# Performance work log

Hardware: AMD Instinct MI355X
Metric: run time of the kernel (lower is better)

Reference implementation:

```python
import jax, jax.numpy as jnp
import numpy as np

B, SEQ, DIM = 32, 512, 1024
DEPTH, HEADS, DHEAD = 6, 8, 64
INNER = HEADS * DHEAD  # 512
NLAT, MAXSEQ = 64, 512
EPS = 1e-5


def setup_inputs() -> dict:
    key = jax.random.key(0)
    ks = jax.random.split(key, 8)
    return {
        "x": jax.random.normal(ks[0], (B, SEQ, DIM), dtype=jnp.float32),
        "attention_mask": jax.random.randint(ks[1], (B, SEQ), 0, 2, dtype=jnp.int32),
        "latents": jax.random.normal(ks[2], (NLAT, DIM), dtype=jnp.float32),
        "media_pos_emb": jax.random.normal(ks[3], (MAXSEQ, DIM), dtype=jnp.float32),
        "ln_media_g": jnp.ones((DEPTH, DIM), jnp.float32),
        "ln_media_b": jnp.zeros((DEPTH, DIM), jnp.float32),
        "ln_lat_g": jnp.ones((DEPTH, DIM), jnp.float32),
        "ln_lat_b": jnp.zeros((DEPTH, DIM), jnp.float32),
        "Wq": jax.random.normal(ks[4], (DEPTH, DIM, INNER), dtype=jnp.float32) * 0.02,
        "Wkv": jax.random.normal(ks[5], (DEPTH, DIM, 2 * INNER), dtype=jnp.float32) * 0.02,
        "Wout": jax.random.normal(ks[6], (DEPTH, INNER, DIM), dtype=jnp.float32) * 0.02,
        "final_g": jnp.ones((DIM,), jnp.float32),
        "final_b": jnp.zeros((DIM,), jnp.float32),
    }


def _layer_norm(x, g, b):
    mu = jnp.mean(x, axis=-1, keepdims=True)
    var = jnp.mean(jnp.square(x - mu), axis=-1, keepdims=True)
    return (x - mu) * jax.lax.rsqrt(var + EPS) * g + b


def _heads(t):
    # b n (h d) -> b h n d
    b, n, _ = t.shape
    return t.reshape(b, n, HEADS, DHEAD).transpose(0, 2, 1, 3)


def reference(x, attention_mask, latents, media_pos_emb, ln_media_g, ln_media_b,
              ln_lat_g, ln_lat_b, Wq, Wkv, Wout, final_g, final_b):
    b, seq, _ = x.shape
    x = x + media_pos_emb[None, :seq, :]
    lat = jnp.broadcast_to(latents[None], (b, NLAT, DIM))
    scale = DHEAD ** -0.5
    # key mask over [latents ++ media]: latent keys never masked; 1 == masked
    key_mask = jnp.concatenate(
        [jnp.zeros((b, NLAT), attention_mask.dtype), attention_mask], axis=1)
    masked = (key_mask == 1)[:, None, None, :]  # b 1 1 j
    for l in range(DEPTH):
        xm = _layer_norm(x, ln_media_g[l], ln_media_b[l])
        ln = _layer_norm(lat, ln_lat_g[l], ln_lat_b[l])
        q = _heads(ln @ Wq[l])                      # b h i d
        kv = jnp.concatenate([ln, xm], axis=1) @ Wkv[l]
        k, v = jnp.split(kv, 2, axis=-1)
        k, v = _heads(k), _heads(v)                 # b h j d
        sim = jnp.einsum('bhid,bhjd->bhij', q * scale, k)
        sim = jnp.where(masked, -jnp.inf, sim)
        attn = jax.nn.softmax(sim, axis=-1)
        out = jnp.einsum('bhij,bhjd->bhid', attn, v)
        out = out.transpose(0, 2, 1, 3).reshape(b, NLAT, INNER)
        lat = lat + out @ Wout[l]
    return _layer_norm(lat, final_g, final_b)
```

## Files before the change

### kernel.cpp

```cpp
#include <hip/hip_runtime.h>
#include <cstdint>


#define DEVINL __device__ __forceinline__

typedef __attribute__((ext_vector_type(8))) short short8_t;
typedef __attribute__((ext_vector_type(4))) float f32x4;

DEVINL ushort f2bf(float f) {
  union { float f; uint32_t u; } c; c.f = f;
  uint32_t u = c.u;
  u += ((u >> 16) & 1u) + 0x7fffu;
  return (ushort)(u >> 16);
}
DEVINL float bf2f(ushort u) {
  union { uint32_t u; float f; } c; c.u = ((uint32_t)u) << 16;
  return c.f;
}
DEVINL f32x4 mfma16(short8_t a, short8_t b, f32x4 c) {
  return __builtin_amdgcn_mfma_f32_16x16x32_bf16(a, b, c, 0, 0, 0);
}
DEVINL void gld16(ushort* lds, const ushort* g) {
  __builtin_amdgcn_global_load_lds(
      (const __attribute__((address_space(1))) void*)g,
      (__attribute__((address_space(3))) void*)lds, 16, 0, 0);
}

__global__ __launch_bounds__(512, 2) void k_gemm256m(const ushort* __restrict__ A,
    const ushort* __restrict__ Bt, const float* __restrict__ bias,
    ushort* __restrict__ Kb, ushort* __restrict__ Vt) {
  extern __shared__ char lds[];
  constexpr int K = 1024, NT = 16;
  int tid = threadIdx.x, lane = tid & 63, w = tid >> 6;
  int wm = w >> 2, wn = w & 3;
  int fr = lane & 15;
  int fkb = (lane >> 4) << 4;
  int xorv = (fr & 7) << 4;
  int bid = blockIdx.x;
  int xcd = bid & 7, ii = bid >> 3;
  int m0 = (xcd * 8 + (ii >> 2)) * 256;
  int n0 = (ii & 3) * 256;
  int srow = w * 8 + (lane >> 3);
  int sce = ((lane & 7) ^ (lane >> 3)) << 3;
  const ushort* Ag = A + (size_t)(m0 + srow) * K + sce;
  const ushort* Bg = Bt + (size_t)(n0 + srow) * K + sce;
  f32x4 acc[8][4] = {};

  auto stA = [&](int t, int h) {
    ushort* d = (ushort*)(lds + (t % 3) * 32768 + h * 16384 + w * 1024);
    const ushort* s = Ag + (size_t)(h * 128) * K + t * 64;
    gld16(d, s);
    gld16((ushort*)((char*)d + 8192), s + (size_t)64 * K);
  };
  auto stB = [&](int t, int h) {
    ushort* d = (ushort*)(lds + 98304 + (t & 1) * 32768 + h * 16384 + w * 1024);
    const ushort* s = Bg + (size_t)(h * 128) * K + t * 64;
    gld16(d, s);
    gld16((ushort*)((char*)d + 8192), s + (size_t)64 * K);
  };
  stA(0, 0); stA(0, 1); stB(0, 0); stB(0, 1); stA(1, 0); stA(1, 1);

#define RD_AFR(DST, MQ)                                                        \
  _Pragma("unroll") for (int m2 = 0; m2 < 2; ++m2)                             \
    _Pragma("unroll") for (int kh = 0; kh < 2; ++kh)                           \
      DST[m2][kh] = *(const short8_t*)(ab +                                    \
          ((wm * 128 + (MQ + m2) * 16 + fr) << 7) + ((kh * 64 + fkb) ^ xorv));

#define CLUSTER(MQ, AFR)                                                       \
  __builtin_amdgcn_s_setprio(1);                                               \
  _Pragma("unroll") for (int kh = 0; kh < 2; ++kh)                             \
    _Pragma("unroll") for (int m2 = 0; m2 < 2; ++m2)                           \
      _Pragma("unroll") for (int nt = 0; nt < 4; ++nt)                         \
        acc[MQ + m2][nt] = mfma16(AFR[m2][kh], bfr[nt][kh], acc[MQ + m2][nt]); \
  __builtin_amdgcn_s_setprio(0);                                               \
  __builtin_amdgcn_s_barrier();

  for (int t = 0; t < NT; ++t) {
    const char* ab = lds + (t % 3) * 32768;
    const char* bb = lds + 98304 + (t & 1) * 32768;
    short8_t bfr[4][2], afrX[2][2], afrY[2][2];
    if (t + 1 < NT) asm volatile("s_waitcnt vmcnt(4)" ::: "memory");
    else            asm volatile("s_waitcnt vmcnt(0)" ::: "memory");
    __builtin_amdgcn_s_barrier();
#pragma unroll
    for (int nt = 0; nt < 4; ++nt)
#pragma unroll
      for (int kh = 0; kh < 2; ++kh)
        bfr[nt][kh] = *(const short8_t*)(bb +
            ((wn * 64 + nt * 16 + fr) << 7) + ((kh * 64 + fkb) ^ xorv));
    RD_AFR(afrX, 0);
    if (t + 1 < NT) stB(t + 1, 0);
    RD_AFR(afrY, 2);
    CLUSTER(0, afrX);
    if (t + 1 < NT) stB(t + 1, 1);
    RD_AFR(afrX, 4);
    CLUSTER(2, afrY);
    if (t + 2 < NT) stA(t + 2, 0);
    RD_AFR(afrY, 6);
    CLUSTER(4, afrX);
    if (t + 2 < NT) stA(t + 2, 1);
    CLUSTER(6, afrY);
  }
#undef RD_AFR
#undef CLUSTER

  __syncthreads();
  ushort* Cl = (ushort*)lds;
  constexpr int CLS = 264;
  for (int p = 0; p < 2; ++p) {
    if (p) __syncthreads();
    if (wm == p) {
#pragma unroll
      for (int mt = 0; mt < 8; ++mt)
#pragma unroll
        for (int nt = 0; nt < 4; ++nt)
#pragma unroll
          for (int r = 0; r < 4; ++r) {
            int rl = mt * 16 + ((lane >> 4) << 2) + r;
            int cl = wn * 64 + nt * 16 + (lane & 15);
            Cl[rl * CLS + cl] = f2bf(acc[mt][nt][r] + bias[n0 + cl]);
          }
    }
    __syncthreads();
    int rowg0 = m0 + p * 128;
    int b_ = rowg0 >> 9;
    int jbase = 64 + (rowg0 & 511);
    if (n0 < 512) {
#pragma unroll
      for (int q2 = 0; q2 < 8; ++q2) {
        int task = tid + q2 * 512;
        int rl = task >> 5, ck = task & 31;
        short8_t vv = *(const short8_t*)&Cl[rl * CLS + ck * 8];
        *(short8_t*)&Kb[((size_t)(b_ * 576 + jbase + rl) << 9) + n0 + ck * 8] = vv;
      }
    } else {
#pragma unroll
      for (int q2 = 0; q2 < 8; ++q2) {
        int task = tid + q2 * 512;
        int d = task >> 4, jg = task & 15;
        short8_t vv;
#pragma unroll
        for (int e = 0; e < 8; ++e) vv[e] = (short)Cl[(jg * 8 + e) * CLS + d];
        *(short8_t*)&Vt[((size_t)(b_ * 512 + (n0 - 512) + d)) * 576 +
                        jbase + jg * 8] = vv;
      }
    }
  }
}

__global__ __launch_bounds__(256) void k_fold_kv(const float* __restrict__ Wkv,
    const float* __restrict__ lnmg, const float* __restrict__ lnlg,
    const float* __restrict__ lnmb, const float* __restrict__ lnlb,
    ushort* __restrict__ wkvmT, ushort* __restrict__ wlatT,
    float* __restrict__ bkvm, float* __restrict__ blat) {
  __shared__ float tile[32][33];
  __shared__ float pm[8][32], pl[8][32];
  int l = blockIdx.y;
  int c0 = blockIdx.x * 32;
  const float* Wl = Wkv + (size_t)l * 1048576;
  int tx = threadIdx.x & 31, ty = threadIdx.x >> 5;
  float am = 0.f, al = 0.f;
  for (int rt = 0; rt < 32; ++rt) {
    int r0 = rt * 32;
    __syncthreads();
#pragma unroll
    for (int i = 0; i < 4; ++i)
      tile[ty + i * 8][tx] = Wl[(size_t)(r0 + ty + i * 8) * 1024 + c0 + tx];
    __syncthreads();
#pragma unroll
    for (int i = 0; i < 4; ++i) {
      int r = ty * 4 + i;
      float wv = tile[r][tx];
      am += lnmb[l * 1024 + r0 + r] * wv;
      al += lnlb[l * 1024 + r0 + r] * wv;
    }
#pragma unroll
    for (int i = 0; i < 4; ++i) {
      int c = ty + i * 8;
      float wv = tile[tx][c];
      int r = r0 + tx;
      wkvmT[(size_t)l * 1048576 + (size_t)(c0 + c) * 1024 + r] =
          f2bf(wv * lnmg[l * 1024 + r]);
      wlatT[(size_t)l * 1572864 + (size_t)(512 + c0 + c) * 1024 + r] =
          f2bf(wv * lnlg[l * 1024 + r]);
    }
  }
  pm[ty][tx] = am; pl[ty][tx] = al;
  __syncthreads();
  if (ty == 0) {
    float sm = 0.f, sl = 0.f;
#pragma unroll
    for (int k = 0; k < 8; ++k) { sm += pm[k][tx]; sl += pl[k][tx]; }
    bkvm[l * 1024 + c0 + tx] = sm;
    blat[l * 1536 + 512 + c0 + tx] = sl;
  }
}

__global__ __launch_bounds__(256) void k_fold_q(const float* __restrict__ Wq,
    const float* __restrict__ lnlg, const float* __restrict__ lnlb,
    ushort* __restrict__ wlatT, float* __restrict__ blat) {
  __shared__ float tile[32][33];
  __shared__ float pq[8][32];
  int l = blockIdx.y;
  int c0 = blockIdx.x * 32;
  const float* Wl = Wq + (size_t)l * 524288;
  int tx = threadIdx.x & 31, ty = threadIdx.x >> 5;
  float aq = 0.f;
  for (int rt = 0; rt < 32; ++rt) {
    int r0 = rt * 32;
    __syncthreads();
#pragma unroll
    for (int i = 0; i < 4; ++i)
      tile[ty + i * 8][tx] = Wl[(size_t)(r0 + ty + i * 8) * 512 + c0 + tx];
    __syncthreads();
#pragma unroll
    for (int i = 0; i < 4; ++i) {
      int r = ty * 4 + i;
      aq += lnlb[l * 1024 + r0 + r] * tile[r][tx];
    }
#pragma unroll
    for (int i = 0; i < 4; ++i) {
      int c = ty + i * 8;
      float wv = tile[tx][c];
      int r = r0 + tx;
      wlatT[(size_t)l * 1572864 + (size_t)(c0 + c) * 1024 + r] =
          f2bf(wv * lnlg[l * 1024 + r] * 0.125f);
    }
  }
  pq[ty][tx] = aq;
  __syncthreads();
  if (ty == 0) {
    float s = 0.f;
#pragma unroll
    for (int k = 0; k < 8; ++k) s += pq[k][tx];
    blat[l * 1536 + c0 + tx] = s * 0.125f;
  }
}

__global__ __launch_bounds__(256) void k_fold_out(const float* __restrict__ Wout,
    ushort* __restrict__ woutT) {
  __shared__ float tile[32][33];
  int l = blockIdx.z;
  const float* Wl = Wout + (size_t)l * 524288;
  int r0 = blockIdx.y * 32, c0 = blockIdx.x * 32;
  int tx = threadIdx.x & 31, ty = threadIdx.x >> 5;
#pragma unroll
  for (int i = 0; i < 4; ++i)
    tile[ty + i * 8][tx] = Wl[(size_t)(r0 + ty + i * 8) * 1024 + c0 + tx];
  __syncthreads();
#pragma unroll
  for (int i = 0; i < 4; ++i) {
    int jl = ty + i * 8;
    woutT[(size_t)l * 524288 + (size_t)(c0 + jl) * 512 + r0 + tx] = f2bf(tile[tx][jl]);
  }
}

__global__ __launch_bounds__(256) void k_rownorm(const float* __restrict__ in,
    const float* __restrict__ pos, ushort* __restrict__ out) {
  int row = blockIdx.x, t = threadIdx.x;
  float4 v = *(const float4*)(in + (size_t)row * 1024 + t * 4);
  if (pos) {
    float4 p = *(const float4*)(pos + (size_t)(row & 511) * 1024 + t * 4);
    v.x += p.x; v.y += p.y; v.z += p.z; v.w += p.w;
  }
  float s = v.x + v.y + v.z + v.w;
  float q = v.x * v.x + v.y * v.y + v.z * v.z + v.w * v.w;
#pragma unroll
  for (int off = 32; off; off >>= 1) { s += __shfl_xor(s, off); q += __shfl_xor(q, off); }
  __shared__ float rs[4], rq[4];
  if ((t & 63) == 0) { rs[t >> 6] = s; rq[t >> 6] = q; }
  __syncthreads();
  s = rs[0] + rs[1] + rs[2] + rs[3];
  q = rq[0] + rq[1] + rq[2] + rq[3];
  float mean = s * (1.0f / 1024.0f);
  float var = q * (1.0f / 1024.0f) - mean * mean;
  float rstd = rsqrtf(var + 1e-5f);
  ushort4 o;
  o.x = f2bf((v.x - mean) * rstd);
  o.y = f2bf((v.y - mean) * rstd);
  o.z = f2bf((v.z - mean) * rstd);
  o.w = f2bf((v.w - mean) * rstd);
  *(ushort4*)(out + (size_t)row * 1024 + t * 4) = o;
}

__global__ __launch_bounds__(256) void k_finalln(const float* __restrict__ in,
    const float* __restrict__ g, const float* __restrict__ b, float* __restrict__ out) {
  int row = blockIdx.x, t = threadIdx.x;
  float4 v = *(const float4*)(in + (size_t)row * 1024 + t * 4);
  float s = v.x + v.y + v.z + v.w;
  float q = v.x * v.x + v.y * v.y + v.z * v.z + v.w * v.w;
#pragma unroll
  for (int off = 32; off; off >>= 1) { s += __shfl_xor(s, off); q += __shfl_xor(q, off); }
  __shared__ float rs[4], rq[4];
  if ((t & 63) == 0) { rs[t >> 6] = s; rq[t >> 6] = q; }
  __syncthreads();
  s = rs[0] + rs[1] + rs[2] + rs[3];
  q = rq[0] + rq[1] + rq[2] + rq[3];
  float mean = s * (1.0f / 1024.0f);
  float var = q * (1.0f / 1024.0f) - mean * mean;
  float rstd = rsqrtf(var + 1e-5f);
  float4 g4 = *(const float4*)(g + t * 4);
  float4 b4 = *(const float4*)(b + t * 4);
  float4 o;
  o.x = (v.x - mean) * rstd * g4.x + b4.x;
  o.y = (v.y - mean) * rstd * g4.y + b4.y;
  o.z = (v.z - mean) * rstd * g4.z + b4.z;
  o.w = (v.w - mean) * rstd * g4.w + b4.w;
  *(float4*)(out + (size_t)row * 1024 + t * 4) = o;
}

__global__ __launch_bounds__(256) void k_latinit(const float* __restrict__ latents,
                                                 float* __restrict__ lat) {
  int row = blockIdx.x, t = threadIdx.x;
  *(float4*)(lat + (size_t)row * 1024 + t * 4) =
      *(const float4*)(latents + (size_t)(row & 63) * 1024 + t * 4);
}

template <int MODE>
__global__ __launch_bounds__(256) void k_gemm64(const ushort* __restrict__ A,
    const ushort* __restrict__ Bt, const float* __restrict__ bias,
    ushort* __restrict__ o0, ushort* __restrict__ o1, ushort* __restrict__ o2,
    float* __restrict__ of, int N, int K) {
  __shared__ ushort Al[2][64][32];
  __shared__ ushort Bl[2][64][32];
  __shared__ ushort Cl[64][72];
  int tid = threadIdx.x, lane = tid & 63, w = tid >> 6;
  int wr = w >> 1, wc = w & 1;
  int m0 = blockIdx.y * 64, n0 = blockIdx.x * 64;
  f32x4 acc[2][2] = {};
  const ushort* Ag = A + (size_t)(m0 + w * 16 + (lane >> 2)) * K + (lane & 3) * 8;
  const ushort* Bg = Bt + (size_t)(n0 + w * 16 + (lane >> 2)) * K + (lane & 3) * 8;
  int fr = lane & 15, fk = (lane >> 4) << 3;
  int nt = K >> 5;
  gld16(&Al[0][w * 16][0], Ag);
  gld16(&Bl[0][w * 16][0], Bg);
  __syncthreads();
  for (int t = 0; t < nt; ++t) {
    int cur = t & 1;
    if (t + 1 < nt) {
      int k0 = (t + 1) << 5;
      gld16(&Al[cur ^ 1][w * 16][0], Ag + k0);
      gld16(&Bl[cur ^ 1][w * 16][0], Bg + k0);
    }
    short8_t a[2], b[2];
#pragma unroll
    for (int mt = 0; mt < 2; ++mt)
      a[mt] = *(const short8_t*)&Al[cur][wr * 32 + mt * 16 + fr][fk];
#pragma unroll
    for (int nt2 = 0; nt2 < 2; ++nt2)
      b[nt2] = *(const short8_t*)&Bl[cur][wc * 32 + nt2 * 16 + fr][fk];
#pragma unroll
    for (int mt = 0; mt < 2; ++mt)
#pragma unroll
      for (int nt2 = 0; nt2 < 2; ++nt2)
        acc[mt][nt2] = mfma16(a[mt], b[nt2], acc[mt][nt2]);
    __syncthreads();
  }
  if constexpr (MODE == 3) {
    if (n0 >= 1024) {
#pragma unroll
      for (int mt = 0; mt < 2; ++mt)
#pragma unroll
        for (int nt2 = 0; nt2 < 2; ++nt2)
#pragma unroll
          for (int r = 0; r < 4; ++r) {
            int rl = wr * 32 + mt * 16 + ((lane >> 4) << 2) + r;
            int col = wc * 32 + nt2 * 16 + (lane & 15);
            Cl[rl][col] = f2bf(acc[mt][nt2][r] + bias[n0 + col]);
          }
      __syncthreads();
      int b_ = m0 >> 6;
#pragma unroll
      for (int q = 0; q < 2; ++q) {
        int task = tid + q * 256;
        int jg = task & 7, d = task >> 3;
        short8_t vv;
#pragma unroll
        for (int e = 0; e < 8; ++e) vv[e] = (short)Cl[jg * 8 + e][d];
        *(short8_t*)&o2[((size_t)(b_ * 512 + (n0 - 1024) + d)) * 576 + jg * 8] = vv;
      }
      return;
    }
  }
#pragma unroll
  for (int mt = 0; mt < 2; ++mt)
#pragma unroll
    for (int nt2 = 0; nt2 < 2; ++nt2)
#pragma unroll
      for (int r = 0; r < 4; ++r) {
        int row = m0 + wr * 32 + mt * 16 + ((lane >> 4) << 2) + r;
        int col = n0 + wc * 32 + nt2 * 16 + (lane & 15);
        float v = acc[mt][nt2][r] + (bias ? bias[col] : 0.0f);
        if constexpr (MODE == 3) {
          int b_ = row >> 6, ii = row & 63;
          if (col < 512) o0[(size_t)row * 512 + col] = f2bf(v);
          else           o1[(((size_t)(b_ * 576 + ii)) << 9) + (col - 512)] = f2bf(v);
        } else {
          of[(size_t)row * N + col] += v;
        }
      }
}

__global__ __launch_bounds__(256) void k_attn(const ushort* __restrict__ Q,
    const ushort* __restrict__ Kb, const ushort* __restrict__ Vt,
    const int* __restrict__ amask, ushort* __restrict__ AO) {
  __shared__ ushort sim[32][584];
  int blk = blockIdx.x;
  int half = blk & 1, h = (blk >> 1) & 7, b = blk >> 4;
  int tid = threadIdx.x, lane = tid & 63, w = tid >> 6;
  int wr = w >> 1, wc = w & 1;
  short8_t aq0, aq1;
  {
    int qi = half * 32 + wr * 16 + (lane & 15);
    const ushort* qp = Q + ((size_t)(b * 64 + qi) << 9) + h * 64 + ((lane >> 4) << 3);
    aq0 = *(const short8_t*)qp;
    aq1 = *(const short8_t*)(qp + 32);
  }
  const ushort* kbase = Kb + (((size_t)(b * 576)) << 9) + h * 64 + ((lane >> 4) << 3);
  for (int jt = 0; jt < 9; ++jt) {
#pragma unroll
    for (int c2 = 0; c2 < 2; ++c2) {
      int ct = wc * 2 + c2;
      const ushort* kp = kbase + (((size_t)(jt * 64 + ct * 16 + (lane & 15))) << 9);
      short8_t bk0 = *(const short8_t*)kp;
      short8_t bk1 = *(const short8_t*)(kp + 32);
      f32x4 acc = {};
      acc = mfma16(aq0, bk0, acc);
      acc = mfma16(aq1, bk1, acc);
#pragma unroll
      for (int r = 0; r < 4; ++r)
        sim[wr * 16 + ((lane >> 4) << 2) + r][jt * 64 + ct * 16 + (lane & 15)] =
            f2bf(acc[r]);
    }
  }
  __syncthreads();
  unsigned mbits = 0;
#pragma unroll
  for (int c = 1; c < 9; ++c)
    if (amask[b * 512 + (c - 1) * 64 + lane]) mbits |= (1u << c);
  for (int rr = 0; rr < 8; ++rr) {
    int row = w * 8 + rr;
    float vals[9];
    float m = -3.0e38f;
#pragma unroll
    for (int c = 0; c < 9; ++c) {
      float v = bf2f(sim[row][c * 64 + lane]);
      vals[c] = v;
      if (!((mbits >> c) & 1)) m = fmaxf(m, v);
    }
#pragma unroll
    for (int off = 32; off; off >>= 1) m = fmaxf(m, __shfl_xor(m, off));
    float ssum = 0.f;
    float p[9];
#pragma unroll
    for (int c = 0; c < 9; ++c) {
      p[c] = ((mbits >> c) & 1) ? 0.f : __expf(vals[c] - m);
      ssum += p[c];
    }
#pragma unroll
    for (int off = 32; off; off >>= 1) ssum += __shfl_xor(ssum, off);
    float inv = 1.0f / ssum;
#pragma unroll
    for (int c = 0; c < 9; ++c)
      sim[row][c * 64 + lane] = f2bf(p[c] * inv);
  }
  __syncthreads();
  f32x4 oacc[2] = {};
  const ushort* vbase = Vt + ((size_t)(b * 512 + h * 64)) * 576 + ((lane >> 4) << 3);
  for (int jt = 0; jt < 9; ++jt) {
    short8_t pa0 = *(const short8_t*)&sim[wr * 16 + (lane & 15)][jt * 64 + ((lane >> 4) << 3)];
    short8_t pa1 = *(const short8_t*)&sim[wr * 16 + (lane & 15)][jt * 64 + 32 + ((lane >> 4) << 3)];
#pragma unroll
    for (int d2 = 0; d2 < 2; ++d2) {
      int dt = wc * 2 + d2;
      const ushort* vp = vbase + (size_t)(dt * 16 + (lane & 15)) * 576 + jt * 64;
      short8_t bv0 = *(const short8_t*)vp;
      short8_t bv1 = *(const short8_t*)(vp + 32);
      oacc[d2] = mfma16(pa0, bv0, oacc[d2]);
      oacc[d2] = mfma16(pa1, bv1, oacc[d2]);
    }
  }
#pragma unroll
  for (int d2 = 0; d2 < 2; ++d2) {
    int dt = wc * 2 + d2;
#pragma unroll
    for (int r = 0; r < 4; ++r) {
      int i = half * 32 + wr * 16 + ((lane >> 4) << 2) + r;
      int d = dt * 16 + (lane & 15);
      AO[((size_t)(b * 64 + i) << 9) + h * 64 + d] = f2bf(oacc[d2][r]);
    }
  }
}

extern "C" void kernel_launch(void* const* d_in, const int* in_sizes, int n_in,
                              void* d_out, int out_size, void* d_ws, size_t ws_size,
                              hipStream_t stream) {
  const float* x       = (const float*)d_in[0];
  const int*   amask   = (const int*)d_in[1];
  const float* latents = (const float*)d_in[2];
  const float* pos     = (const float*)d_in[3];
  const float* lnmg    = (const float*)d_in[4];
  const float* lnmb    = (const float*)d_in[5];
  const float* lnlg    = (const float*)d_in[6];
  const float* lnlb    = (const float*)d_in[7];
  const float* Wq      = (const float*)d_in[8];
  const float* Wkv     = (const float*)d_in[9];
  const float* Wout    = (const float*)d_in[10];
  const float* fg      = (const float*)d_in[11];
  const float* fb      = (const float*)d_in[12];
  float* out = (float*)d_out;
  char* ws = (char*)d_ws;

  ushort* xhat  = (ushort*)(ws + 0);
  ushort* wkvmT = (ushort*)(ws + 33554432);
  ushort* wlatT = (ushort*)(ws + 46137344);
  ushort* woutT = (ushort*)(ws + 65011712);
  float*  bkvm  = (float*)(ws + 71303168);
  float*  blat  = (float*)(ws + 71327744);
  float*  lat   = (float*)(ws + 71364608);
  ushort* lhat  = (ushort*)(ws + 79753216);
  ushort* qbuf  = (ushort*)(ws + 83947520);
  ushort* Kbuf  = (ushort*)(ws + 86044672);
  ushort* Vt    = (ushort*)(ws + 104919040);
  ushort* aobuf = (ushort*)(ws + 123793408);

  (void)hipFuncSetAttribute((const void*)k_gemm256m,
                            hipFuncAttributeMaxDynamicSharedMemorySize, 163840);

  dim3 B256(256);
  k_fold_kv<<<dim3(32, 6), B256, 0, stream>>>(Wkv, lnmg, lnlg, lnmb, lnlb,
                                              wkvmT, wlatT, bkvm, blat);
  k_fold_q<<<dim3(16, 6), B256, 0, stream>>>(Wq, lnlg, lnlb, wlatT, blat);
  k_fold_out<<<dim3(32, 16, 6), B256, 0, stream>>>(Wout, woutT);
  k_rownorm<<<16384, B256, 0, stream>>>(x, pos, xhat);
  k_latinit<<<2048, B256, 0, stream>>>(latents, lat);

  for (int l = 0; l < 6; ++l) {
    k_rownorm<<<2048, B256, 0, stream>>>(lat, nullptr, lhat);
    k_gemm64<3><<<dim3(24, 32), B256, 0, stream>>>(
        lhat, wlatT + (size_t)l * 1572864, blat + l * 1536,
        qbuf, Kbuf, Vt, nullptr, 1536, 1024);
    k_gemm256m<<<dim3(256), dim3(512), 163840, stream>>>(
        xhat, wkvmT + (size_t)l * 1048576, bkvm + l * 1024, Kbuf, Vt);
    k_attn<<<512, B256, 0, stream>>>(qbuf, Kbuf, Vt, amask, aobuf);
    k_gemm64<2><<<dim3(16, 32), B256, 0, stream>>>(
        aobuf, woutT + (size_t)l * 524288, nullptr,
        nullptr, nullptr, nullptr, lat, 1024, 512);
  }
  k_finalln<<<2048, B256, 0, stream>>>(lat, fg, fb, out);
}
```

Baseline: 737.9 us.

## Stage K/V through swizzled LDS with double buffering in attention, single-pass GEMM epilogue

The attention kernel now runs one 512-thread block per (batch, head) instead of splitting query rows across two blocks. K and V tiles are staged into XOR-swizzled shared memory with async global-to-LDS loads, double buffered so loads overlap the MFMA work. This removes the duplicated K/V global reads and the strided per-lane loads of the old version. Separately, the KV GEMM epilogue writes the whole 256-row tile to LDS in one pass, transposing on the write for V instead of on the read, which halves the barriers and makes V stores contiguous. In exchange, grid size drops to 256 blocks and each block uses about 121 KB of LDS, which lowers occupancy.

```diff
diff --git a/kernel.cpp b/kernel.cpp
--- a/kernel.cpp
+++ b/kernel.cpp
@@ -107,45 +107,170 @@
   __syncthreads();
   ushort* Cl = (ushort*)lds;
   constexpr int CLS = 264;
-  for (int p = 0; p < 2; ++p) {
-    if (p) __syncthreads();
-    if (wm == p) {
-#pragma unroll
-      for (int mt = 0; mt < 8; ++mt)
-#pragma unroll
-        for (int nt = 0; nt < 4; ++nt)
-#pragma unroll
-          for (int r = 0; r < 4; ++r) {
-            int rl = mt * 16 + ((lane >> 4) << 2) + r;
-            int cl = wn * 64 + nt * 16 + (lane & 15);
-            Cl[rl * CLS + cl] = f2bf(acc[mt][nt][r] + bias[n0 + cl]);
-          }
-    }
-    __syncthreads();
-    int rowg0 = m0 + p * 128;
-    int b_ = rowg0 >> 9;
-    int jbase = 64 + (rowg0 & 511);
-    if (n0 < 512) {
-#pragma unroll
-      for (int q2 = 0; q2 < 8; ++q2) {
-        int task = tid + q2 * 512;
-        int rl = task >> 5, ck = task & 31;
-        short8_t vv = *(const short8_t*)&Cl[rl * CLS + ck * 8];
-        *(short8_t*)&Kb[((size_t)(b_ * 576 + jbase + rl) << 9) + n0 + ck * 8] = vv;
+  bool isV = (n0 >= 512);
+#pragma unroll
+  for (int mt = 0; mt < 8; ++mt)
+#pragma unroll
+    for (int nt = 0; nt < 4; ++nt)
+#pragma unroll
+      for (int r = 0; r < 4; ++r) {
+        int rl = wm * 128 + mt * 16 + ((lane >> 4) << 2) + r;
+        int cl = wn * 64 + nt * 16 + fr;
+        ushort v = f2bf(acc[mt][nt][r] + bias[n0 + cl]);
+        if (!isV) Cl[rl * CLS + cl] = v;
+        else      Cl[cl * CLS + rl] = v;
       }
+  __syncthreads();
+  int b_ = m0 >> 9;
+  int jb = 64 + (m0 & 511);
+#pragma unroll
+  for (int q2 = 0; q2 < 16; ++q2) {
+    int task = tid + q2 * 512;
+    int rr2 = task >> 5, c8 = task & 31;
+    short8_t vv = *(const short8_t*)&Cl[rr2 * CLS + c8 * 8];
+    if (!isV)
+      *(short8_t*)&Kb[((size_t)(b_ * 576 + jb + rr2) << 9) + n0 + c8 * 8] = vv;
+    else
+      *(short8_t*)&Vt[(size_t)(b_ * 512 + (n0 - 512) + rr2) * 576 + jb + c8 * 8] = vv;
+  }
+}
+
+__global__ __launch_bounds__(512) void k_attn(const ushort* __restrict__ Q,
+    const ushort* __restrict__ Kb, const ushort* __restrict__ Vt,
+    const int* __restrict__ amask, ushort* __restrict__ AO) {
+  extern __shared__ char alds[];
+  ushort* sim = (ushort*)alds;
+  char* stg = alds + 74752;
+  int bh = blockIdx.x;
+  int h = bh & 7, b = bh >> 3;
+  int tid = threadIdx.x, lane = tid & 63, w = tid >> 6;
+  int rg = w >> 1, ch = w & 1;
+  int fr = lane & 15;
+  int fkb = (lane >> 4) << 4;
+  int csrc8 = ((lane & 7) ^ (lane >> 3)) << 3;
+  short8_t aq0, aq1;
+  {
+    int qi = rg * 16 + fr;
+    const ushort* qp = Q + ((size_t)(b * 64 + qi) << 9) + h * 64 + ((lane >> 4) << 3);
+    aq0 = *(const short8_t*)qp;
+    aq1 = *(const short8_t*)(qp + 32);
+  }
+  unsigned mbits = 0;
+#pragma unroll
+  for (int c = 1; c < 9; ++c)
+    if (amask[b * 512 + (c - 1) * 64 + lane]) mbits |= (1u << c);
+
+  auto stageK = [&](int it, int buf) {
+#pragma unroll
+    for (int g = 0; g < 3; ++g) {
+      int sr = w * 24 + g * 8 + (lane >> 3);
+      ushort* d = (ushort*)(stg + buf * 24576 + (w * 24 + g * 8) * 128);
+      gld16(d, Kb + ((size_t)(b * 576 + it * 192 + sr) << 9) + h * 64 + csrc8);
+    }
+  };
+  auto stageV = [&](int it, int buf) {
+#pragma unroll
+    for (int g = 0; g < 3; ++g) {
+      int sr = w * 8 + (lane >> 3);
+      ushort* d = (ushort*)(stg + buf * 24576 + g * 8192 + w * 8 * 128);
+      gld16(d, Vt + (size_t)(b * 512 + h * 64 + sr) * 576 + it * 192 + g * 64 + csrc8);
+    }
+  };
+
+  stageK(0, 0);
+  for (int it = 0; it < 3; ++it) {
+    int buf = it & 1;
+    __builtin_amdgcn_s_barrier();
+    if (it + 1 < 3) {
+      stageK(it + 1, buf ^ 1);
+      asm volatile("s_waitcnt vmcnt(3)" ::: "memory");
     } else {
-#pragma unroll
-      for (int q2 = 0; q2 < 8; ++q2) {
-        int task = tid + q2 * 512;
-        int d = task >> 4, jg = task & 15;
-        short8_t vv;
-#pragma unroll
-        for (int e = 0; e < 8; ++e) vv[e] = (short)Cl[(jg * 8 + e) * CLS + d];
-        *(short8_t*)&Vt[((size_t)(b_ * 512 + (n0 - 512) + d)) * 576 +
-                        jbase + jg * 8] = vv;
+      asm volatile("s_waitcnt vmcnt(0)" ::: "memory");
+    }
+    __builtin_amdgcn_s_barrier();
+    const char* kb_ = stg + buf * 24576;
+#pragma unroll
+    for (int ct = 0; ct < 6; ++ct) {
+      int row_l = ch * 96 + ct * 16 + fr;
+      const char* base = kb_ + row_l * 128;
+      int sw = (row_l & 7) << 4;
+      short8_t k0 = *(const short8_t*)(base + (fkb ^ sw));
+      short8_t k1 = *(const short8_t*)(base + ((64 + fkb) ^ sw));
+      f32x4 s4 = {};
+      s4 = mfma16(aq0, k0, s4);
+      s4 = mfma16(aq1, k1, s4);
+#pragma unroll
+      for (int r = 0; r < 4; ++r)
+        sim[(rg * 16 + ((lane >> 4) << 2) + r) * 584 +
+            it * 192 + ch * 96 + ct * 16 + fr] = f2bf(s4[r]);
+    }
+  }
+  __syncthreads();
+  for (int rr = 0; rr < 8; ++rr) {
+    int row = w * 8 + rr;
+    float vals[9];
+    float m = -3.0e38f;
+#pragma unroll
+    for (int c = 0; c < 9; ++c) {
+      float v = bf2f(sim[row * 584 + c * 64 + lane]);
+      vals[c] = v;
+      if (!((mbits >> c) & 1)) m = fmaxf(m, v);
+    }
+#pragma unroll
+    for (int off = 32; off; off >>= 1) m = fmaxf(m, __shfl_xor(m, off));
+    float ssum = 0.f;
+    float p[9];
+#pragma unroll
+    for (int c = 0; c < 9; ++c) {
+      p[c] = ((mbits >> c) & 1) ? 0.f : __expf(vals[c] - m);
+      ssum += p[c];
+    }
+#pragma unroll
+    for (int off = 32; off; off >>= 1) ssum += __shfl_xor(ssum, off);
+    float inv = 1.0f / ssum;
+#pragma unroll
+    for (int c = 0; c < 9; ++c)
+      sim[row * 584 + c * 64 + lane] = f2bf(p[c] * inv);
+  }
+  __syncthreads();
+  f32x4 oacc[2] = {};
+  stageV(0, 0);
+  for (int it = 0; it < 3; ++it) {
+    int buf = it & 1;
+    __builtin_amdgcn_s_barrier();
+    if (it + 1 < 3) {
+      stageV(it + 1, buf ^ 1);
+      asm volatile("s_waitcnt vmcnt(3)" ::: "memory");
+    } else {
+      asm volatile("s_waitcnt vmcnt(0)" ::: "memory");
+    }
+    __builtin_amdgcn_s_barrier();
+#pragma unroll
+    for (int g = 0; g < 3; ++g) {
+      const char* vb_ = stg + buf * 24576 + g * 8192;
+      const ushort* srow_ = &sim[(rg * 16 + fr) * 584 + it * 192 + g * 64];
+      short8_t pa0 = *(const short8_t*)(srow_ + ((lane >> 4) << 3));
+      short8_t pa1 = *(const short8_t*)(srow_ + 32 + ((lane >> 4) << 3));
+#pragma unroll
+      for (int dt = 0; dt < 2; ++dt) {
+        int row_l = ch * 32 + dt * 16 + fr;
+        const char* base = vb_ + row_l * 128;
+        int sw = (row_l & 7) << 4;
+        short8_t v0 = *(const short8_t*)(base + (fkb ^ sw));
+        short8_t v1 = *(const short8_t*)(base + ((64 + fkb) ^ sw));
+        oacc[dt] = mfma16(pa0, v0, oacc[dt]);
+        oacc[dt] = mfma16(pa1, v1, oacc[dt]);
       }
     }
   }
+#pragma unroll
+  for (int dt = 0; dt < 2; ++dt)
+#pragma unroll
+    for (int r = 0; r < 4; ++r) {
+      int i = rg * 16 + ((lane >> 4) << 2) + r;
+      int d = ch * 32 + dt * 16 + fr;
+      AO[((size_t)(b * 64 + i) << 9) + h * 64 + d] = f2bf(oacc[dt][r]);
+    }
 }
 
 __global__ __launch_bounds__(256) void k_fold_kv(const float* __restrict__ Wkv,
@@ -401,97 +526,6 @@
       }
 }
 
-__global__ __launch_bounds__(256) void k_attn(const ushort* __restrict__ Q,
-    const ushort* __restrict__ Kb, const ushort* __restrict__ Vt,
-    const int* __restrict__ amask, ushort* __restrict__ AO) {
-  __shared__ ushort sim[32][584];
-  int blk = blockIdx.x;
-  int half = blk & 1, h = (blk >> 1) & 7, b = blk >> 4;
-  int tid = threadIdx.x, lane = tid & 63, w = tid >> 6;
-  int wr = w >> 1, wc = w & 1;
-  short8_t aq0, aq1;
-  {
-    int qi = half * 32 + wr * 16 + (lane & 15);
-    const ushort* qp = Q + ((size_t)(b * 64 + qi) << 9) + h * 64 + ((lane >> 4) << 3);
-    aq0 = *(const short8_t*)qp;
-    aq1 = *(const short8_t*)(qp + 32);
-  }
-  const ushort* kbase = Kb + (((size_t)(b * 576)) << 9) + h * 64 + ((lane >> 4) << 3);
-  for (int jt = 0; jt < 9; ++jt) {
-#pragma unroll
-    for (int c2 = 0; c2 < 2; ++c2) {
-      int ct = wc * 2 + c2;
-      const ushort* kp = kbase + (((size_t)(jt * 64 + ct * 16 + (lane & 15))) << 9);
-      short8_t bk0 = *(const short8_t*)kp;
-      short8_t bk1 = *(const short8_t*)(kp + 32);
-      f32x4 acc = {};
-      acc = mfma16(aq0, bk0, acc);
-      acc = mfma16(aq1, bk1, acc);
-#pragma unroll
-      for (int r = 0; r < 4; ++r)
-        sim[wr * 16 + ((lane >> 4) << 2) + r][jt * 64 + ct * 16 + (lane & 15)] =
-            f2bf(acc[r]);
-    }
-  }
-  __syncthreads();
-  unsigned mbits = 0;
-#pragma unroll
-  for (int c = 1; c < 9; ++c)
-    if (amask[b * 512 + (c - 1) * 64 + lane]) mbits |= (1u << c);
-  for (int rr = 0; rr < 8; ++rr) {
-    int row = w * 8 + rr;
-    float vals[9];
-    float m = -3.0e38f;
-#pragma unroll
-    for (int c = 0; c < 9; ++c) {
-      float v = bf2f(sim[row][c * 64 + lane]);
-      vals[c] = v;
-      if (!((mbits >> c) & 1)) m = fmaxf(m, v);
-    }
-#pragma unroll
-    for (int off = 32; off; off >>= 1) m = fmaxf(m, __shfl_xor(m, off));
-    float ssum = 0.f;
-    float p[9];
-#pragma unroll
-    for (int c = 0; c < 9; ++c) {
-      p[c] = ((mbits >> c) & 1) ? 0.f : __expf(vals[c] - m);
-      ssum += p[c];
-    }
-#pragma unroll
-    for (int off = 32; off; off >>= 1) ssum += __shfl_xor(ssum, off);
-    float inv = 1.0f / ssum;
-#pragma unroll
-    for (int c = 0; c < 9; ++c)
-      sim[row][c * 64 + lane] = f2bf(p[c] * inv);
-  }
-  __syncthreads();
-  f32x4 oacc[2] = {};
-  const ushort* vbase = Vt + ((size_t)(b * 512 + h * 64)) * 576 + ((lane >> 4) << 3);
-  for (int jt = 0; jt < 9; ++jt) {
-    short8_t pa0 = *(const short8_t*)&sim[wr * 16 + (lane & 15)][jt * 64 + ((lane >> 4) << 3)];
-    short8_t pa1 = *(const short8_t*)&sim[wr * 16 + (lane & 15)][jt * 64 + 32 + ((lane >> 4) << 3)];
-#pragma unroll
-    for (int d2 = 0; d2 < 2; ++d2) {
-      int dt = wc * 2 + d2;
-      const ushort* vp = vbase + (size_t)(dt * 16 + (lane & 15)) * 576 + jt * 64;
-      short8_t bv0 = *(const short8_t*)vp;
-      short8_t bv1 = *(const short8_t*)(vp + 32);
-      oacc[d2] = mfma16(pa0, bv0, oacc[d2]);
-      oacc[d2] = mfma16(pa1, bv1, oacc[d2]);
-    }
-  }
-#pragma unroll
-  for (int d2 = 0; d2 < 2; ++d2) {
-    int dt = wc * 2 + d2;
-#pragma unroll
-    for (int r = 0; r < 4; ++r) {
-      int i = half * 32 + wr * 16 + ((lane >> 4) << 2) + r;
-      int d = dt * 16 + (lane & 15);
-      AO[((size_t)(b * 64 + i) << 9) + h * 64 + d] = f2bf(oacc[d2][r]);
-    }
-  }
-}
-
 extern "C" void kernel_launch(void* const* d_in, const int* in_sizes, int n_in,
                               void* d_out, int out_size, void* d_ws, size_t ws_size,
                               hipStream_t stream) {
@@ -526,6 +560,8 @@
 
   (void)hipFuncSetAttribute((const void*)k_gemm256m,
                             hipFuncAttributeMaxDynamicSharedMemorySize, 163840);
+  (void)hipFuncSetAttribute((const void*)k_attn,
+                            hipFuncAttributeMaxDynamicSharedMemorySize, 131072);
 
   dim3 B256(256);
   k_fold_kv<<<dim3(32, 6), B256, 0, stream>>>(Wkv, lnmg, lnlg, lnmb, lnlb,
@@ -542,7 +578,7 @@
         qbuf, Kbuf, Vt, nullptr, 1536, 1024);
     k_gemm256m<<<dim3(256), dim3(512), 163840, stream>>>(
         xhat, wkvmT + (size_t)l * 1048576, bkvm + l * 1024, Kbuf, Vt);
-    k_attn<<<512, B256, 0, stream>>>(qbuf, Kbuf, Vt, amask, aobuf);
+    k_attn<<<dim3(256), dim3(512), 123904, stream>>>(qbuf, Kbuf, Vt, amask, aobuf);
     k_gemm64<2><<<dim3(16, 32), B256, 0, stream>>>(
         aobuf, woutT + (size_t)l * 524288, nullptr,
         nullptr, nullptr, nullptr, lat, 1024, 512);
```

New measurement: 643.4 us. -12.8%, faster.
